# Performance work log

Hardware: AMD Instinct MI355X
Metric: run time of the kernel (lower is better)

The kernel has to match this reference:

```python
import jax, jax.numpy as jnp
import numpy as np

RARITY_ALPHA = 0.5


def _forward(obs_emb, observed_mask, lengths, avg_interval, var_prior_emb_tensor,
             rarity_W, adjI, p2s_W1, p2s_b1, p2s_W2, p2s_b2,
             Wu, bu, Wr, br, Wc, bc):
    B, T, N, D = obs_emb.shape
    I = jnp.eye(N, dtype=obs_emb.dtype)
    # hypernetwork conditioning vector per node (prior_to_state MLP); identical
    # across batch since var_prior_emb_tensor is repeated over the batch dim.
    vv = jax.nn.relu(var_prior_emb_tensor @ p2s_W1 + p2s_b1) @ p2s_W2 + p2s_b2  # [N,E]
    vv = jnp.broadcast_to(vv[None], (B, N, vv.shape[-1]))                        # [B,N,E]
    tot = observed_mask.sum(axis=1)  # var_total_obs [B,N]

    def gate(z, W, b):
        # MLP_Param: per-node weights W_n = sum_e vv[n,e]*W[e]; fused einsum avoids
        # materializing [B,N,2D+1,D].
        return jnp.einsum('bni,bne,eio->bno', z, vv, W) + jnp.einsum('bne,eo->bno', vv, b)

    def step_fn(carry, xs):
        h, out = carry
        cur_obs, m, cur_avg, step = xs  # [B,N,D], [B,N], [B,N], scalar
        rs = RARITY_ALPHA * jnp.tanh(cur_avg / (tot + 1.0))                  # [B,N]
        rmat = -rarity_W * jnp.abs(rs[:, :, None] - rs[:, None, :])          # [B,N,N]
        # adj_mask[b,i,j] = observed(b,i)*observed(b,j)  (column-set then row-zero)
        adj_mask = m[:, :, None] * m[:, None, :]
        cur_adj = adjI * (1.0 + rmat) * adj_mask * (1.0 - I) + I             # [B,N,N]
        x = jnp.concatenate([cur_obs, rs[..., None]], axis=-1)              # [B,N,D+1]
        comb = jnp.einsum('bij,bjf->bif', cur_adj,
                          jnp.concatenate([x, h], axis=-1))                  # [B,N,2D+1]
        r = jax.nn.sigmoid(gate(comb, Wr, br))
        u = jax.nn.sigmoid(gate(comb, Wu, bu))
        mm = m[..., None] > 0
        h1 = jnp.where(mm, r * h, h)                      # h[nodes_ind] = r*h[nodes_ind]
        cand = jnp.tanh(gate(jnp.concatenate([x, h1], axis=-1), Wc, bc))
        h2 = jnp.where(mm, (1.0 - u) * h1 + u * cand, h1)  # scatter back at observed nodes
        out = jnp.where((step == lengths - 1)[:, None, None], h2, out)
        return (h2, out), None

    h0 = jnp.zeros((B, N, D), obs_emb.dtype)
    xs = (obs_emb.transpose(1, 0, 2, 3), observed_mask.transpose(1, 0, 2),
          avg_interval.transpose(1, 0, 2), jnp.arange(T))
    (_, out), _ = jax.lax.scan(step_fn, (h0, jnp.zeros_like(h0)), xs)
    return out


def setup_inputs() -> dict:
    B, T, N, D, E = 32, 64, 128, 64, 5
    key = jax.random.key(0)
    ks = jax.random.split(key, 18)
    inp = {}
    inp['obs_emb'] = jax.random.normal(ks[0], (B, T, N, D), jnp.float32)
    inp['adj'] = jax.random.normal(ks[1], (N, N), jnp.float32)  # unused by forward
    inp['observed_mask'] = (jax.random.uniform(ks[2], (B, T, N)) < 0.5).astype(jnp.float32)
    inp['observed_tp'] = jax.random.uniform(ks[3], (B, T), jnp.float32)       # unused
    inp['tp_emb_tensor'] = jax.random.normal(ks[4], (B, T, 1), jnp.float32)   # unused
    inp['lengths'] = jax.random.randint(ks[5], (B,), T // 2, T + 1, jnp.int32)
    inp['avg_interval'] = jax.random.uniform(ks[6], (B, T, N), jnp.float32)
    inp['var_prior_emb_tensor'] = jax.random.normal(ks[7], (N, 768), jnp.float32)
    # learned parameters
    inp['rarity_W'] = jax.random.normal(ks[8], (N, N), jnp.float32)
    inp['adjI'] = jnp.eye(N, dtype=jnp.float32) + 0.01 * jax.random.normal(ks[9], (N, N), jnp.float32)
    inp['p2s_W1'] = 0.05 * jax.random.normal(ks[10], (768, 2 * D), jnp.float32)
    inp['p2s_b1'] = jnp.zeros((2 * D,), jnp.float32)
    inp['p2s_W2'] = 0.1 * jax.random.normal(ks[11], (2 * D, E), jnp.float32)
    inp['p2s_b2'] = jnp.zeros((E,), jnp.float32)
    inp['Wu'] = 0.1 * jax.random.normal(ks[12], (E, 2 * D + 1, D), jnp.float32)
    inp['bu'] = 0.1 * jax.random.normal(ks[13], (E, D), jnp.float32)
    inp['Wr'] = 0.1 * jax.random.normal(ks[14], (E, 2 * D + 1, D), jnp.float32)
    inp['br'] = 0.1 * jax.random.normal(ks[15], (E, D), jnp.float32)
    inp['Wc'] = 0.1 * jax.random.normal(ks[16], (E, 2 * D + 1, D), jnp.float32)
    inp['bc'] = 0.1 * jax.random.normal(ks[17], (E, D), jnp.float32)
    return inp


def reference(obs_emb, adj, observed_mask, observed_tp, tp_emb_tensor, lengths,
              avg_interval, var_prior_emb_tensor, rarity_W, adjI, p2s_W1, p2s_b1,
              p2s_W2, p2s_b2, Wu, bu, Wr, br, Wc, bc):
    # adj, observed_tp, tp_emb_tensor are accepted but never used, as in the torch code
    return _forward(obs_emb, observed_mask, lengths, avg_interval, var_prior_emb_tensor,
                    rarity_W, adjI, p2s_W1, p2s_b1, p2s_W2, p2s_b2,
                    Wu, bu, Wr, br, Wc, bc)
```

## Files before the change

### kernel.cpp

```cpp
#include <hip/hip_runtime.h>
#include <math.h>

constexpr size_t WS_VV  = 1024;
constexpr size_t WS_TOT = 2048;
constexpr size_t WS_RS  = 8192;
constexpr size_t WS_WH  = 270336;
constexpr size_t WS_WX  = 1843200;
constexpr size_t WS_BF  = 3440640;
constexpr size_t WS_H   = 3465216;
constexpr size_t WS_CH  = 3727360;
constexpr size_t WS_CX  = 3989504;
constexpr size_t WS_GXR = 8249344;
constexpr size_t WS_GXU = 12443648;
constexpr size_t WS_CXC = 16637952;

__device__ __forceinline__ float sigm(float x){ return 1.f/(1.f+expf(-x)); }

__device__ __forceinline__ float2 ld2_mall(const float* p){
  union { unsigned long long u; float2 f; } cv;
  cv.u = __hip_atomic_load((const unsigned long long*)p, __ATOMIC_RELAXED,
                           __HIP_MEMORY_SCOPE_AGENT);
  return cv.f;
}
__device__ __forceinline__ void st2_mall(float* p, float a, float b){
  union { unsigned long long u; float2 f; } cv;
  cv.f = make_float2(a, b);
  __hip_atomic_store((unsigned long long*)p, cv.u, __ATOMIC_RELAXED,
                     __HIP_MEMORY_SCOPE_AGENT);
}

__global__ void k_vv(const float* __restrict__ vpe, const float* __restrict__ W1,
                     const float* __restrict__ b1, const float* __restrict__ W2,
                     const float* __restrict__ b2, float* __restrict__ ws){
  int n = blockIdx.x, tid = threadIdx.x;
  __shared__ float hid[128];
  if (tid < 128){
    float acc = b1[tid];
    for (int k=0;k<768;k++) acc = fmaf(vpe[n*768+k], W1[k*128+tid], acc);
    hid[tid] = fmaxf(acc, 0.f);
  }
  __syncthreads();
  if (tid < 5){
    float acc = b2[tid];
    for (int h=0;h<128;h++) acc = fmaf(hid[h], W2[h*5+tid], acc);
    ws[WS_VV + n*5 + tid] = acc;
  }
}

__global__ void k_fold(const float* __restrict__ Wr, const float* __restrict__ Wu,
                       const float* __restrict__ Wc, const float* __restrict__ br,
                       const float* __restrict__ bu, const float* __restrict__ bc,
                       float* __restrict__ ws){
  int bid = blockIdx.x; int g = bid>>7; int n = bid&127;
  const float* W  = (g==0)?Wr:(g==1)?Wu:Wc;
  const float* bb = (g==0)?br:(g==1)?bu:bc;
  float v[5];
#pragma unroll
  for (int e=0;e<5;e++) v[e] = ws[WS_VV + n*5 + e];
  for (int idx=threadIdx.x; idx<129*64; idx+=256){
    int i = idx>>6, o = idx&63;
    float a = 0.f;
#pragma unroll
    for (int e=0;e<5;e++) a = fmaf(v[e], W[(e*129+i)*64+o], a);
    if (i < 65) ws[WS_WX + (size_t)(g*128+n)*4160 + i*64 + o] = a;
    else        ws[WS_WH + (size_t)(g*128+n)*4096 + (i-65)*64 + o] = a;
  }
  if (threadIdx.x < 64){
    int o = threadIdx.x; float a = 0.f;
#pragma unroll
    for (int e=0;e<5;e++) a = fmaf(v[e], bb[e*64+o], a);
    ws[WS_BF + (g*128+n)*64 + o] = a;
  }
}

__global__ void k_tot(const float* __restrict__ mask, float* __restrict__ ws){
  int id = blockIdx.x*256 + threadIdx.x;
  int b = id>>7, n = id&127;
  float s = 0.f;
  for (int t=0;t<64;t++) s += mask[(b*64+t)*128 + n];
  ws[WS_TOT + b*128 + n] = s;
}

__global__ void k_rs(const float* __restrict__ avg, float* __restrict__ ws){
  int id = blockIdx.x*256 + threadIdx.x;
  int b = id>>13, n = id&127;
  float tot = ws[WS_TOT + b*128 + n];
  ws[WS_RS + id] = 0.5f * tanhf(avg[id] / (tot + 1.f));
}

__global__ __launch_bounds__(256) void p4a(const float* __restrict__ obs,
      const float* __restrict__ mask, const float* __restrict__ adjI,
      const float* __restrict__ rW, const int* __restrict__ lengths,
      float* __restrict__ ws, int c0){
  int rc = blockIdx.x;
  int b = rc>>4, tl = rc&15, t = c0 + tl;
  if (t >= lengths[b]) return;
  int rt = b*64 + t;
  __shared__ float xt[64*68];
  __shared__ float adjh[128*68];
  __shared__ float rs_l[128], m_l[128];
  int tid = threadIdx.x;
  if (tid < 128){ rs_l[tid] = ws[WS_RS + rt*128 + tid]; m_l[tid] = mask[rt*128 + tid]; }
  __syncthreads();
  int it = tid>>3, ft = tid&7, i0 = it*4, f0 = ft*8;
  float4 aL[4], aH[4]; float a64[4];
#pragma unroll
  for (int ii=0;ii<4;ii++){ aL[ii]=make_float4(0,0,0,0); aH[ii]=make_float4(0,0,0,0); a64[ii]=0.f; }
  for (int half=0; half<2; half++){
    __syncthreads();
    int j0 = half*64;
    for (int idx=tid; idx<4096; idx+=256){
      int jl = idx>>6, f = idx&63;
      xt[jl*68+f] = obs[(size_t)rt*8192 + (j0+jl)*64 + f];
    }
    if (tid < 64) xt[tid*68+64] = rs_l[j0+tid];
    for (int idx=tid; idx<8192; idx+=256){
      int i = idx>>6, jl = idx&63, j = j0+jl;
      float a;
      if (i == j) a = 1.f;
      else {
        int gi = i*128 + j;
        float dd = fabsf(rs_l[i] - rs_l[j]);
        a = adjI[gi] * (1.f - rW[gi]*dd) * m_l[i] * m_l[j];
      }
      adjh[i*68+jl] = a;
    }
    __syncthreads();
    for (int jb=0; jb<16; jb++){
      float4 av[4];
#pragma unroll
      for (int ii=0;ii<4;ii++) av[ii] = *(const float4*)&adjh[(i0+ii)*68 + jb*4];
#pragma unroll
      for (int jj=0;jj<4;jj++){
        int jl = jb*4 + jj;
        float4 xlo = *(const float4*)&xt[jl*68 + f0];
        float4 xhi = *(const float4*)&xt[jl*68 + f0 + 4];
        float xr = xt[jl*68 + 64];
#pragma unroll
        for (int ii=0;ii<4;ii++){
          float a = (jj==0)?av[ii].x:(jj==1)?av[ii].y:(jj==2)?av[ii].z:av[ii].w;
          aL[ii].x = fmaf(a, xlo.x, aL[ii].x); aL[ii].y = fmaf(a, xlo.y, aL[ii].y);
          aL[ii].z = fmaf(a, xlo.z, aL[ii].z); aL[ii].w = fmaf(a, xlo.w, aL[ii].w);
          aH[ii].x = fmaf(a, xhi.x, aH[ii].x); aH[ii].y = fmaf(a, xhi.y, aH[ii].y);
          aH[ii].z = fmaf(a, xhi.z, aH[ii].z); aH[ii].w = fmaf(a, xhi.w, aH[ii].w);
          a64[ii] = fmaf(a, xr, a64[ii]);
        }
      }
    }
  }
#pragma unroll
  for (int ii=0;ii<4;ii++){
    int i = i0 + ii;
    size_t base = WS_CX + (size_t)i*33280 + (size_t)rc*65 + f0;
    ws[base+0]=aL[ii].x; ws[base+1]=aL[ii].y; ws[base+2]=aL[ii].z; ws[base+3]=aL[ii].w;
    ws[base+4]=aH[ii].x; ws[base+5]=aH[ii].y; ws[base+6]=aH[ii].z; ws[base+7]=aH[ii].w;
    if (ft == 0) ws[WS_CX + (size_t)i*33280 + (size_t)rc*65 + 64] = a64[ii];
  }
}

__global__ __launch_bounds__(256) void p4b(const float* __restrict__ obs,
      const int* __restrict__ lengths, float* __restrict__ ws, int c0){
  int bid = blockIdx.x;
  int g = bid >> 9; int r2 = bid & 511; int n = r2 >> 2; int tile = r2 & 3;
  __shared__ float A[128*69];
  __shared__ float Wl[65*64];
  __shared__ float bl[64];
  __shared__ int slen[32];
  int tid = threadIdx.x;
  if (tid < 32) slen[tid] = lengths[tid];
  for (int idx=tid; idx<4160; idx+=256) Wl[idx] = ws[WS_WX + (size_t)(g*128+n)*4160 + idx];
  if (tid < 64) bl[tid] = ws[WS_BF + (g*128+n)*64 + tid];
  if (g < 2){
    const float* src = &ws[WS_CX + (size_t)n*33280 + (size_t)tile*8320];
    for (int idx=tid; idx<8320; idx+=256){
      int r = idx/65, f = idx - r*65;
      A[r*69+f] = src[idx];
    }
  } else {
    for (int idx=tid; idx<8320; idx+=256){
      int r = idx/65, f = idx - r*65;
      int grow = tile*128 + r;
      int gb = grow>>4, t = c0 + (grow&15);
      float v = (f < 64) ? obs[(size_t)(gb*64+t)*8192 + n*64 + f]
                         : ws[WS_RS + (gb*64+t)*128 + n];
      A[r*69+f] = v;
    }
  }
  __syncthreads();
  int rt8 = tid>>4, dq = tid&15;
  float4 acc[8];
#pragma unroll
  for (int rr=0;rr<8;rr++) acc[rr] = make_float4(0,0,0,0);
  for (int k=0;k<65;k++){
    float4 w = *(const float4*)&Wl[k*64 + dq*4];
#pragma unroll
    for (int rr=0;rr<8;rr++){
      float a = A[(rt8*8+rr)*69 + k];
      acc[rr].x = fmaf(a,w.x,acc[rr].x); acc[rr].y = fmaf(a,w.y,acc[rr].y);
      acc[rr].z = fmaf(a,w.z,acc[rr].z); acc[rr].w = fmaf(a,w.w,acc[rr].w);
    }
  }
  float4 b4 = *(const float4*)&bl[dq*4];
  float* dst = &ws[(g==0)?WS_GXR:(g==1)?WS_GXU:WS_CXC];
#pragma unroll
  for (int rr=0;rr<8;rr++){
    int grow = tile*128 + rt8*8 + rr;
    int gb = grow>>4, gtl = grow&15;
    if (c0 + gtl < slen[gb]){
      float4 o; o.x=acc[rr].x+b4.x; o.y=acc[rr].y+b4.y; o.z=acc[rr].z+b4.z; o.w=acc[rr].w+b4.w;
      *(float4*)&dst[((size_t)(n*16+gtl)*32 + gb)*64 + dq*4] = o;
    }
  }
}

__global__ __launch_bounds__(256) void krec(const float* __restrict__ mask,
      const int* __restrict__ lengths, const float* __restrict__ adjI,
      const float* __restrict__ rWm, float* __restrict__ out, float* __restrict__ ws,
      int c0){
  unsigned* cfl = (unsigned*)ws;
  unsigned* hfl = ((unsigned*)ws) + 256;
  const int bid = blockIdx.x, tid = threadIdx.x;
  const int bA = bid>>3, sA = bid&7, ns = sA*16;
  const int nB = bid>>1, hf = bid&1, b0 = hf*16;
  __shared__ float hs[8192];
  __shared__ float adjT[2560];
  __shared__ float cT[1088];
  __shared__ float hT[1088];
  __shared__ float rs_l[128], m_l[128];
  const int lenA = lengths[bA];
  const int il = tid>>4, fq = tid&15;
  const int bb = b0 + il;
  const int slenB = lengths[bb];
  float* hbuf = &ws[WS_H];
  float* chb  = &ws[WS_CH];
  const float* wrg = &ws[WS_WH + (size_t)(0*128+nB)*4096];
  const float* wug = &ws[WS_WH + (size_t)(1*128+nB)*4096];
  const float* wcg = &ws[WS_WH + (size_t)(2*128+nB)*4096];
  float4 hst;
  { const float* hp = &hbuf[((size_t)bb*128+nB)*64 + fq*4];
    float2 lo = ld2_mall(hp), hi = ld2_mall(hp+2);
    hst = make_float4(lo.x, lo.y, hi.x, hi.y); }

  for (int t=c0; t<c0+16; t++){
    const int tl = t - c0;
    const bool aliveA = (t < lenA);
    const bool aliveB = (t < slenB);
    if (aliveA){
      if (tid < 128) rs_l[tid] = ws[WS_RS + (size_t)(bA*64+t)*128 + tid];
      else           m_l[tid-128] = mask[(size_t)(bA*64+t)*128 + (tid-128)];
    }
    __syncthreads();
    if (aliveA){
      for (int idx=tid; idx<2048; idx+=256){
        int j = idx&127, r = idx>>7, I = ns+r;
        float a;
        if (I == j) a = 1.f;
        else {
          int gi = I*128 + j;
          float dd = fabsf(rs_l[I] - rs_l[j]);
          a = adjI[gi]*(1.f - rWm[gi]*dd)*m_l[I]*m_l[j];
        }
        adjT[j*20 + r] = a;
      }
    }
    float4 arv, auv, acv; float msv = 0.f;
    if (aliveB){
      size_t gof = ((size_t)(nB*16+tl)*32 + bb)*64 + fq*4;
      arv = *(const float4*)&ws[WS_GXR + gof];
      auv = *(const float4*)&ws[WS_GXU + gof];
      acv = *(const float4*)&ws[WS_CXC + gof];
      msv = mask[(size_t)(bb*64+t)*128 + nB];
    }
    if (aliveA && t > 0 && tid < 128){
      unsigned tgt = (unsigned)t; int guard = 0;
      while (__hip_atomic_load(&hfl[tid*2 + (bA>>4)], __ATOMIC_RELAXED,
               __HIP_MEMORY_SCOPE_AGENT) < tgt && ++guard < (1<<20))
        __builtin_amdgcn_s_sleep(1);
    }
    __syncthreads();
    if (aliveA){
#pragma unroll
      for (int k2=0;k2<16;k2++){
        int p = tid + 256*k2;
        float2 v = ld2_mall(&hbuf[(size_t)bA*8192 + 2*p]);
        *(float2*)&hs[2*p] = v;
      }
    }
    __syncthreads();
    if (aliveA && tid < 128){
      int pr = tid>>4;
      float4 a0 = make_float4(0,0,0,0), a1 = a0;
#pragma unroll 4
      for (int j=0;j<128;j++){
        float2 aj = *(const float2*)&adjT[j*20 + pr*2];
        float4 h4 = *(const float4*)&hs[j*64 + fq*4];
        a0.x = fmaf(aj.x,h4.x,a0.x); a0.y = fmaf(aj.x,h4.y,a0.y);
        a0.z = fmaf(aj.x,h4.z,a0.z); a0.w = fmaf(aj.x,h4.w,a0.w);
        a1.x = fmaf(aj.y,h4.x,a1.x); a1.y = fmaf(aj.y,h4.y,a1.y);
        a1.z = fmaf(aj.y,h4.z,a1.z); a1.w = fmaf(aj.y,h4.w,a1.w);
      }
      float* cp0 = &chb[((size_t)bA*128 + ns + pr*2)*64 + fq*4];
      st2_mall(cp0,    a0.x, a0.y); st2_mall(cp0+2,  a0.z, a0.w);
      st2_mall(cp0+64, a1.x, a1.y); st2_mall(cp0+66, a1.z, a1.w);
    }
    __syncthreads();
    if (tid == 0)
      __hip_atomic_store(&cfl[sA*32 + bA], (unsigned)(t+1), __ATOMIC_RELAXED,
                         __HIP_MEMORY_SCOPE_AGENT);
    if (aliveB && fq == 0){
      unsigned tgt = (unsigned)(t+1); int guard = 0;
      while (__hip_atomic_load(&cfl[(nB>>4)*32 + bb], __ATOMIC_RELAXED,
               __HIP_MEMORY_SCOPE_AGENT) < tgt && ++guard < (1<<20))
        __builtin_amdgcn_s_sleep(1);
    }
    __syncthreads();
    if (aliveB){
      const float* cp = &chb[((size_t)bb*128 + nB)*64 + fq*4];
      float2 u = ld2_mall(cp), v = ld2_mall(cp+2);
      cT[il*68 + fq*4    ] = u.x; cT[il*68 + fq*4 + 1] = u.y;
      cT[il*68 + fq*4 + 2] = v.x; cT[il*68 + fq*4 + 3] = v.y;
    }
    __syncthreads();
    float4 uu, h1v;
    const bool ob = msv > 0.f;
    if (aliveB){
#pragma unroll 4
      for (int k=0;k<64;k++){
        float cv = cT[il*68 + k];
        float4 wr4 = *(const float4*)&wrg[k*64 + fq*4];
        float4 wu4 = *(const float4*)&wug[k*64 + fq*4];
        arv.x = fmaf(cv,wr4.x,arv.x); arv.y = fmaf(cv,wr4.y,arv.y);
        arv.z = fmaf(cv,wr4.z,arv.z); arv.w = fmaf(cv,wr4.w,arv.w);
        auv.x = fmaf(cv,wu4.x,auv.x); auv.y = fmaf(cv,wu4.y,auv.y);
        auv.z = fmaf(cv,wu4.z,auv.z); auv.w = fmaf(cv,wu4.w,auv.w);
      }
      float4 rr;
      rr.x = sigm(arv.x); rr.y = sigm(arv.y); rr.z = sigm(arv.z); rr.w = sigm(arv.w);
      uu.x = sigm(auv.x); uu.y = sigm(auv.y); uu.z = sigm(auv.z); uu.w = sigm(auv.w);
      h1v.x = ob ? rr.x*hst.x : hst.x;
      h1v.y = ob ? rr.y*hst.y : hst.y;
      h1v.z = ob ? rr.z*hst.z : hst.z;
      h1v.w = ob ? rr.w*hst.w : hst.w;
      *(float4*)&hT[il*68 + fq*4] = h1v;
    }
    __syncthreads();
    if (aliveB){
#pragma unroll 4
      for (int k=0;k<64;k++){
        float hv = hT[il*68 + k];
        float4 wc4 = *(const float4*)&wcg[k*64 + fq*4];
        acv.x = fmaf(hv,wc4.x,acv.x); acv.y = fmaf(hv,wc4.y,acv.y);
        acv.z = fmaf(hv,wc4.z,acv.z); acv.w = fmaf(hv,wc4.w,acv.w);
      }
      float4 cd, h2;
      cd.x = tanhf(acv.x); cd.y = tanhf(acv.y); cd.z = tanhf(acv.z); cd.w = tanhf(acv.w);
      h2.x = ob ? (1.f-uu.x)*h1v.x + uu.x*cd.x : h1v.x;
      h2.y = ob ? (1.f-uu.y)*h1v.y + uu.y*cd.y : h1v.y;
      h2.z = ob ? (1.f-uu.z)*h1v.z + uu.z*cd.z : h1v.z;
      h2.w = ob ? (1.f-uu.w)*h1v.w + uu.w*cd.w : h1v.w;
      hst = h2;
      float* hp = &hbuf[((size_t)bb*128 + nB)*64 + fq*4];
      st2_mall(hp,   h2.x, h2.y);
      st2_mall(hp+2, h2.z, h2.w);
      if (t == slenB-1)
        *(float4*)&out[((size_t)bb*128 + nB)*64 + fq*4] = h2;
    }
    __syncthreads();
    if (tid == 0)
      __hip_atomic_store(&hfl[nB*2 + hf], (unsigned)(t+1), __ATOMIC_RELAXED,
                         __HIP_MEMORY_SCOPE_AGENT);
  }
}

extern "C" void kernel_launch(void* const* d_in, const int* in_sizes, int n_in,
                              void* d_out, int out_size, void* d_ws, size_t ws_size,
                              hipStream_t stream){
  const float* obs  = (const float*)d_in[0];
  const float* maskp= (const float*)d_in[2];
  const int*   lens = (const int*)d_in[5];
  const float* avg  = (const float*)d_in[6];
  const float* vpe  = (const float*)d_in[7];
  const float* rW   = (const float*)d_in[8];
  const float* adjI = (const float*)d_in[9];
  const float* W1   = (const float*)d_in[10];
  const float* b1   = (const float*)d_in[11];
  const float* W2   = (const float*)d_in[12];
  const float* b2   = (const float*)d_in[13];
  const float* Wu   = (const float*)d_in[14];
  const float* bu   = (const float*)d_in[15];
  const float* Wr   = (const float*)d_in[16];
  const float* br   = (const float*)d_in[17];
  const float* Wc   = (const float*)d_in[18];
  const float* bc   = (const float*)d_in[19];
  float* out = (float*)d_out;
  float* ws  = (float*)d_ws;
  hipMemsetAsync(d_ws, 0, 4096, stream);
  hipMemsetAsync((char*)d_ws + WS_H*sizeof(float), 0, 262144*sizeof(float), stream);
  k_vv  <<<128, 256, 0, stream>>>(vpe, W1, b1, W2, b2, ws);
  k_fold<<<384, 256, 0, stream>>>(Wr, Wu, Wc, br, bu, bc, ws);
  k_tot <<<16,  256, 0, stream>>>(maskp, ws);
  k_rs  <<<1024,256, 0, stream>>>(avg, ws);
  for (int c = 0; c < 4; c++){
    int c0 = c*16;
    p4a <<<512, 256, 0, stream>>>(obs, maskp, adjI, rW, lens, ws, c0);
    p4b <<<1536,256, 0, stream>>>(obs, lens, ws, c0);
    krec<<<256, 256, 0, stream>>>(maskp, lens, adjI, rW, out, ws, c0);
  }
}
```

Before: 1.675 ms.

## Split recurrent kernel into separate aggregation and gate block roles

The persistent recurrent kernel now launches 512 blocks: the first 256 compute the adjacency aggregation and publish results, and the other 256 compute the per-node GRU gates. Each gate block caches its three per-node weight matrices in shared memory once per chunk and has each thread handle two batch rows. Stores are drained with an explicit waitcnt before the flag is published. The aim is to pipeline the two phases across blocks and cut repeated global weight reads. The cost is more blocks spinning on flags, half the threads idle in gate blocks, and a risk of deadlock if all 512 blocks are not co-resident.

```diff
diff --git a/kernel.cpp b/kernel.cpp
--- a/kernel.cpp
+++ b/kernel.cpp
@@ -220,155 +220,202 @@
   unsigned* cfl = (unsigned*)ws;
   unsigned* hfl = ((unsigned*)ws) + 256;
   const int bid = blockIdx.x, tid = threadIdx.x;
-  const int bA = bid>>3, sA = bid&7, ns = sA*16;
-  const int nB = bid>>1, hf = bid&1, b0 = hf*16;
-  __shared__ float hs[8192];
-  __shared__ float adjT[2560];
-  __shared__ float cT[1088];
-  __shared__ float hT[1088];
-  __shared__ float rs_l[128], m_l[128];
-  const int lenA = lengths[bA];
-  const int il = tid>>4, fq = tid&15;
-  const int bb = b0 + il;
-  const int slenB = lengths[bb];
+  __shared__ float smem[14848];
   float* hbuf = &ws[WS_H];
   float* chb  = &ws[WS_CH];
-  const float* wrg = &ws[WS_WH + (size_t)(0*128+nB)*4096];
-  const float* wug = &ws[WS_WH + (size_t)(1*128+nB)*4096];
-  const float* wcg = &ws[WS_WH + (size_t)(2*128+nB)*4096];
-  float4 hst;
-  { const float* hp = &hbuf[((size_t)bb*128+nB)*64 + fq*4];
-    float2 lo = ld2_mall(hp), hi = ld2_mall(hp+2);
-    hst = make_float4(lo.x, lo.y, hi.x, hi.y); }
-
-  for (int t=c0; t<c0+16; t++){
-    const int tl = t - c0;
-    const bool aliveA = (t < lenA);
-    const bool aliveB = (t < slenB);
-    if (aliveA){
-      if (tid < 128) rs_l[tid] = ws[WS_RS + (size_t)(bA*64+t)*128 + tid];
-      else           m_l[tid-128] = mask[(size_t)(bA*64+t)*128 + (tid-128)];
-    }
+
+  if (bid < 256){
+    const int bA = bid>>3, sA = bid&7, ns = sA*16;
+    float* hs   = smem;
+    float* adjT = smem + 8192;
+    float* rs_l = smem + 10752;
+    float* m_l  = smem + 10880;
+    const int lenA = lengths[bA];
+    const int pr = tid>>4, fq = tid&15;
+    for (int t=c0; t<c0+16; t++){
+      const bool aliveA = (t < lenA);
+      if (aliveA){
+        if (tid < 128) rs_l[tid] = ws[WS_RS + (size_t)(bA*64+t)*128 + tid];
+        else           m_l[tid-128] = mask[(size_t)(bA*64+t)*128 + (tid-128)];
+      }
+      __syncthreads();
+      if (aliveA){
+        for (int idx=tid; idx<2048; idx+=256){
+          int j = idx&127, r = idx>>7, I = ns+r;
+          float a;
+          if (I == j) a = 1.f;
+          else {
+            int gi = I*128 + j;
+            float dd = fabsf(rs_l[I] - rs_l[j]);
+            a = adjI[gi]*(1.f - rWm[gi]*dd)*m_l[I]*m_l[j];
+          }
+          adjT[j*20 + r] = a;
+        }
+        if (t > 0 && tid < 128){
+          unsigned tgt = (unsigned)t; int guard = 0;
+          while (__hip_atomic_load(&hfl[tid*2 + (bA>>4)], __ATOMIC_RELAXED,
+                   __HIP_MEMORY_SCOPE_AGENT) < tgt && ++guard < (1<<20))
+            __builtin_amdgcn_s_sleep(1);
+        }
+      }
+      __syncthreads();
+      if (aliveA){
+#pragma unroll
+        for (int k2=0;k2<16;k2++){
+          int p = tid + 256*k2;
+          float2 v = ld2_mall(&hbuf[(size_t)bA*8192 + 2*p]);
+          *(float2*)&hs[2*p] = v;
+        }
+      }
+      __syncthreads();
+      if (aliveA && tid < 128){
+        float4 a0 = make_float4(0,0,0,0), a1 = a0;
+#pragma unroll 4
+        for (int j=0;j<128;j++){
+          float2 aj = *(const float2*)&adjT[j*20 + pr*2];
+          float4 h4 = *(const float4*)&hs[j*64 + fq*4];
+          a0.x = fmaf(aj.x,h4.x,a0.x); a0.y = fmaf(aj.x,h4.y,a0.y);
+          a0.z = fmaf(aj.x,h4.z,a0.z); a0.w = fmaf(aj.x,h4.w,a0.w);
+          a1.x = fmaf(aj.y,h4.x,a1.x); a1.y = fmaf(aj.y,h4.y,a1.y);
+          a1.z = fmaf(aj.y,h4.z,a1.z); a1.w = fmaf(aj.y,h4.w,a1.w);
+        }
+        float* cp0 = &chb[((size_t)bA*128 + ns + pr*2)*64 + fq*4];
+        st2_mall(cp0,    a0.x, a0.y); st2_mall(cp0+2,  a0.z, a0.w);
+        st2_mall(cp0+64, a1.x, a1.y); st2_mall(cp0+66, a1.z, a1.w);
+      }
+      asm volatile("s_waitcnt vmcnt(0)" ::: "memory");
+      __syncthreads();
+      if (tid == 0)
+        __hip_atomic_store(&cfl[sA*32 + bA], (unsigned)(t+1), __ATOMIC_RELAXED,
+                           __HIP_MEMORY_SCOPE_AGENT);
+    }
+  } else {
+    const int nB = (bid-256)>>1, hf = (bid-256)&1, b0 = hf*16;
+    float* wR = smem;
+    float* wU = smem + 4096;
+    float* wC = smem + 8192;
+    float* cT = smem + 12288;
+    float* hT = smem + 13568;
+    for (int idx=tid; idx<3072; idx+=256){
+      int g = idx>>10, r = idx&1023;
+      *(float4*)&smem[g*4096 + r*4] =
+        *(const float4*)&ws[WS_WH + (size_t)(g*128+nB)*4096 + (size_t)r*4];
+    }
+    const int p = tid>>4, fq = tid&15;
+    const int bb0 = b0 + ((p&7)*2), bb1 = bb0 + 1;
+    const int sl0 = lengths[bb0], sl1 = lengths[bb1];
+    float4 h0, h1p;
+    { const float* q0 = &hbuf[((size_t)bb0*128+nB)*64 + fq*4];
+      const float* q1 = &hbuf[((size_t)bb1*128+nB)*64 + fq*4];
+      float2 a = ld2_mall(q0), b = ld2_mall(q0+2);
+      float2 c = ld2_mall(q1), d = ld2_mall(q1+2);
+      h0 = make_float4(a.x,a.y,b.x,b.y); h1p = make_float4(c.x,c.y,d.x,d.y); }
     __syncthreads();
-    if (aliveA){
-      for (int idx=tid; idx<2048; idx+=256){
-        int j = idx&127, r = idx>>7, I = ns+r;
-        float a;
-        if (I == j) a = 1.f;
-        else {
-          int gi = I*128 + j;
-          float dd = fabsf(rs_l[I] - rs_l[j]);
-          a = adjI[gi]*(1.f - rWm[gi]*dd)*m_l[I]*m_l[j];
-        }
-        adjT[j*20 + r] = a;
-      }
-    }
-    float4 arv, auv, acv; float msv = 0.f;
-    if (aliveB){
-      size_t gof = ((size_t)(nB*16+tl)*32 + bb)*64 + fq*4;
-      arv = *(const float4*)&ws[WS_GXR + gof];
-      auv = *(const float4*)&ws[WS_GXU + gof];
-      acv = *(const float4*)&ws[WS_CXC + gof];
-      msv = mask[(size_t)(bb*64+t)*128 + nB];
-    }
-    if (aliveA && t > 0 && tid < 128){
-      unsigned tgt = (unsigned)t; int guard = 0;
-      while (__hip_atomic_load(&hfl[tid*2 + (bA>>4)], __ATOMIC_RELAXED,
-               __HIP_MEMORY_SCOPE_AGENT) < tgt && ++guard < (1<<20))
-        __builtin_amdgcn_s_sleep(1);
-    }
-    __syncthreads();
-    if (aliveA){
-#pragma unroll
-      for (int k2=0;k2<16;k2++){
-        int p = tid + 256*k2;
-        float2 v = ld2_mall(&hbuf[(size_t)bA*8192 + 2*p]);
-        *(float2*)&hs[2*p] = v;
-      }
-    }
-    __syncthreads();
-    if (aliveA && tid < 128){
-      int pr = tid>>4;
-      float4 a0 = make_float4(0,0,0,0), a1 = a0;
+    for (int t=c0; t<c0+16; t++){
+      const int tl = t - c0;
+      const bool al0 = (t < sl0), al1 = (t < sl1);
+      float4 xr0,xr1,xu0,xu1,xc0,xc1; float m0=0.f, m1=0.f;
+      if (tid < 128){
+        size_t g0 = ((size_t)(nB*16+tl)*32 + bb0)*64 + fq*4;
+        size_t g1 = ((size_t)(nB*16+tl)*32 + bb1)*64 + fq*4;
+        xr0 = *(const float4*)&ws[WS_GXR + g0]; xr1 = *(const float4*)&ws[WS_GXR + g1];
+        xu0 = *(const float4*)&ws[WS_GXU + g0]; xu1 = *(const float4*)&ws[WS_GXU + g1];
+        xc0 = *(const float4*)&ws[WS_CXC + g0]; xc1 = *(const float4*)&ws[WS_CXC + g1];
+        m0 = mask[(size_t)(bb0*64+t)*128 + nB];
+        m1 = mask[(size_t)(bb1*64+t)*128 + nB];
+      }
+      if (tid < 16){
+        unsigned tgt = (unsigned)(t+1); int guard = 0;
+        while (__hip_atomic_load(&cfl[(nB>>4)*32 + b0 + tid], __ATOMIC_RELAXED,
+                 __HIP_MEMORY_SCOPE_AGENT) < tgt && ++guard < (1<<20))
+          __builtin_amdgcn_s_sleep(1);
+      }
+      __syncthreads();
+      {
+        int bi = tid>>4, fg = tid&15, f0 = fg*4;
+        const float* cp = &chb[((size_t)(b0+bi)*128 + nB)*64 + f0];
+        float2 u = ld2_mall(cp), v = ld2_mall(cp+2);
+        cT[(f0  )*20 + bi] = u.x; cT[(f0+1)*20 + bi] = u.y;
+        cT[(f0+2)*20 + bi] = v.x; cT[(f0+3)*20 + bi] = v.y;
+      }
+      __syncthreads();
+      float4 uu0, uu1, h1a, h1b;
+      const bool ob0 = m0 > 0.f, ob1 = m1 > 0.f;
+      if (tid < 128){
+        float4 ar0=xr0, ar1=xr1, au0=xu0, au1=xu1;
 #pragma unroll 4
-      for (int j=0;j<128;j++){
-        float2 aj = *(const float2*)&adjT[j*20 + pr*2];
-        float4 h4 = *(const float4*)&hs[j*64 + fq*4];
-        a0.x = fmaf(aj.x,h4.x,a0.x); a0.y = fmaf(aj.x,h4.y,a0.y);
-        a0.z = fmaf(aj.x,h4.z,a0.z); a0.w = fmaf(aj.x,h4.w,a0.w);
-        a1.x = fmaf(aj.y,h4.x,a1.x); a1.y = fmaf(aj.y,h4.y,a1.y);
-        a1.z = fmaf(aj.y,h4.z,a1.z); a1.w = fmaf(aj.y,h4.w,a1.w);
-      }
-      float* cp0 = &chb[((size_t)bA*128 + ns + pr*2)*64 + fq*4];
-      st2_mall(cp0,    a0.x, a0.y); st2_mall(cp0+2,  a0.z, a0.w);
-      st2_mall(cp0+64, a1.x, a1.y); st2_mall(cp0+66, a1.z, a1.w);
-    }
-    __syncthreads();
-    if (tid == 0)
-      __hip_atomic_store(&cfl[sA*32 + bA], (unsigned)(t+1), __ATOMIC_RELAXED,
-                         __HIP_MEMORY_SCOPE_AGENT);
-    if (aliveB && fq == 0){
-      unsigned tgt = (unsigned)(t+1); int guard = 0;
-      while (__hip_atomic_load(&cfl[(nB>>4)*32 + bb], __ATOMIC_RELAXED,
-               __HIP_MEMORY_SCOPE_AGENT) < tgt && ++guard < (1<<20))
-        __builtin_amdgcn_s_sleep(1);
-    }
-    __syncthreads();
-    if (aliveB){
-      const float* cp = &chb[((size_t)bb*128 + nB)*64 + fq*4];
-      float2 u = ld2_mall(cp), v = ld2_mall(cp+2);
-      cT[il*68 + fq*4    ] = u.x; cT[il*68 + fq*4 + 1] = u.y;
-      cT[il*68 + fq*4 + 2] = v.x; cT[il*68 + fq*4 + 3] = v.y;
-    }
-    __syncthreads();
-    float4 uu, h1v;
-    const bool ob = msv > 0.f;
-    if (aliveB){
+        for (int k=0;k<64;k++){
+          float2 c2 = *(const float2*)&cT[k*20 + (p&7)*2];
+          float4 wr4 = *(const float4*)&wR[k*64 + fq*4];
+          float4 wu4 = *(const float4*)&wU[k*64 + fq*4];
+          ar0.x = fmaf(c2.x,wr4.x,ar0.x); ar0.y = fmaf(c2.x,wr4.y,ar0.y);
+          ar0.z = fmaf(c2.x,wr4.z,ar0.z); ar0.w = fmaf(c2.x,wr4.w,ar0.w);
+          ar1.x = fmaf(c2.y,wr4.x,ar1.x); ar1.y = fmaf(c2.y,wr4.y,ar1.y);
+          ar1.z = fmaf(c2.y,wr4.z,ar1.z); ar1.w = fmaf(c2.y,wr4.w,ar1.w);
+          au0.x = fmaf(c2.x,wu4.x,au0.x); au0.y = fmaf(c2.x,wu4.y,au0.y);
+          au0.z = fmaf(c2.x,wu4.z,au0.z); au0.w = fmaf(c2.x,wu4.w,au0.w);
+          au1.x = fmaf(c2.y,wu4.x,au1.x); au1.y = fmaf(c2.y,wu4.y,au1.y);
+          au1.z = fmaf(c2.y,wu4.z,au1.z); au1.w = fmaf(c2.y,wu4.w,au1.w);
+        }
+        float4 r0, r1;
+        r0.x=sigm(ar0.x); r0.y=sigm(ar0.y); r0.z=sigm(ar0.z); r0.w=sigm(ar0.w);
+        r1.x=sigm(ar1.x); r1.y=sigm(ar1.y); r1.z=sigm(ar1.z); r1.w=sigm(ar1.w);
+        uu0.x=sigm(au0.x); uu0.y=sigm(au0.y); uu0.z=sigm(au0.z); uu0.w=sigm(au0.w);
+        uu1.x=sigm(au1.x); uu1.y=sigm(au1.y); uu1.z=sigm(au1.z); uu1.w=sigm(au1.w);
+        bool q0 = al0 && ob0, q1 = al1 && ob1;
+        h1a.x = q0 ? r0.x*h0.x : h0.x;  h1a.y = q0 ? r0.y*h0.y : h0.y;
+        h1a.z = q0 ? r0.z*h0.z : h0.z;  h1a.w = q0 ? r0.w*h0.w : h0.w;
+        h1b.x = q1 ? r1.x*h1p.x : h1p.x; h1b.y = q1 ? r1.y*h1p.y : h1p.y;
+        h1b.z = q1 ? r1.z*h1p.z : h1p.z; h1b.w = q1 ? r1.w*h1p.w : h1p.w;
+        const float* pa = (const float*)&h1a;
+        const float* pb = (const float*)&h1b;
+#pragma unroll
+        for (int q=0;q<4;q++)
+          *(float2*)&hT[(fq*4+q)*20 + (p&7)*2] = make_float2(pa[q], pb[q]);
+      }
+      __syncthreads();
+      if (tid < 128){
+        float4 ac0=xc0, ac1=xc1;
 #pragma unroll 4
-      for (int k=0;k<64;k++){
-        float cv = cT[il*68 + k];
-        float4 wr4 = *(const float4*)&wrg[k*64 + fq*4];
-        float4 wu4 = *(const float4*)&wug[k*64 + fq*4];
-        arv.x = fmaf(cv,wr4.x,arv.x); arv.y = fmaf(cv,wr4.y,arv.y);
-        arv.z = fmaf(cv,wr4.z,arv.z); arv.w = fmaf(cv,wr4.w,arv.w);
-        auv.x = fmaf(cv,wu4.x,auv.x); auv.y = fmaf(cv,wu4.y,auv.y);
-        auv.z = fmaf(cv,wu4.z,auv.z); auv.w = fmaf(cv,wu4.w,auv.w);
-      }
-      float4 rr;
-      rr.x = sigm(arv.x); rr.y = sigm(arv.y); rr.z = sigm(arv.z); rr.w = sigm(arv.w);
-      uu.x = sigm(auv.x); uu.y = sigm(auv.y); uu.z = sigm(auv.z); uu.w = sigm(auv.w);
-      h1v.x = ob ? rr.x*hst.x : hst.x;
-      h1v.y = ob ? rr.y*hst.y : hst.y;
-      h1v.z = ob ? rr.z*hst.z : hst.z;
-      h1v.w = ob ? rr.w*hst.w : hst.w;
-      *(float4*)&hT[il*68 + fq*4] = h1v;
-    }
-    __syncthreads();
-    if (aliveB){
-#pragma unroll 4
-      for (int k=0;k<64;k++){
-        float hv = hT[il*68 + k];
-        float4 wc4 = *(const float4*)&wcg[k*64 + fq*4];
-        acv.x = fmaf(hv,wc4.x,acv.x); acv.y = fmaf(hv,wc4.y,acv.y);
-        acv.z = fmaf(hv,wc4.z,acv.z); acv.w = fmaf(hv,wc4.w,acv.w);
-      }
-      float4 cd, h2;
-      cd.x = tanhf(acv.x); cd.y = tanhf(acv.y); cd.z = tanhf(acv.z); cd.w = tanhf(acv.w);
-      h2.x = ob ? (1.f-uu.x)*h1v.x + uu.x*cd.x : h1v.x;
-      h2.y = ob ? (1.f-uu.y)*h1v.y + uu.y*cd.y : h1v.y;
-      h2.z = ob ? (1.f-uu.z)*h1v.z + uu.z*cd.z : h1v.z;
-      h2.w = ob ? (1.f-uu.w)*h1v.w + uu.w*cd.w : h1v.w;
-      hst = h2;
-      float* hp = &hbuf[((size_t)bb*128 + nB)*64 + fq*4];
-      st2_mall(hp,   h2.x, h2.y);
-      st2_mall(hp+2, h2.z, h2.w);
-      if (t == slenB-1)
-        *(float4*)&out[((size_t)bb*128 + nB)*64 + fq*4] = h2;
-    }
-    __syncthreads();
-    if (tid == 0)
-      __hip_atomic_store(&hfl[nB*2 + hf], (unsigned)(t+1), __ATOMIC_RELAXED,
-                         __HIP_MEMORY_SCOPE_AGENT);
+        for (int k=0;k<64;k++){
+          float2 hh = *(const float2*)&hT[k*20 + (p&7)*2];
+          float4 wc4 = *(const float4*)&wC[k*64 + fq*4];
+          ac0.x = fmaf(hh.x,wc4.x,ac0.x); ac0.y = fmaf(hh.x,wc4.y,ac0.y);
+          ac0.z = fmaf(hh.x,wc4.z,ac0.z); ac0.w = fmaf(hh.x,wc4.w,ac0.w);
+          ac1.x = fmaf(hh.y,wc4.x,ac1.x); ac1.y = fmaf(hh.y,wc4.y,ac1.y);
+          ac1.z = fmaf(hh.y,wc4.z,ac1.z); ac1.w = fmaf(hh.y,wc4.w,ac1.w);
+        }
+        if (al0){
+          float4 cd, h2;
+          cd.x=tanhf(ac0.x); cd.y=tanhf(ac0.y); cd.z=tanhf(ac0.z); cd.w=tanhf(ac0.w);
+          h2.x = ob0 ? (1.f-uu0.x)*h1a.x + uu0.x*cd.x : h1a.x;
+          h2.y = ob0 ? (1.f-uu0.y)*h1a.y + uu0.y*cd.y : h1a.y;
+          h2.z = ob0 ? (1.f-uu0.z)*h1a.z + uu0.z*cd.z : h1a.z;
+          h2.w = ob0 ? (1.f-uu0.w)*h1a.w + uu0.w*cd.w : h1a.w;
+          h0 = h2;
+          float* hp = &hbuf[((size_t)bb0*128 + nB)*64 + fq*4];
+          st2_mall(hp, h2.x, h2.y); st2_mall(hp+2, h2.z, h2.w);
+          if (t == sl0-1) *(float4*)&out[((size_t)bb0*128 + nB)*64 + fq*4] = h2;
+        }
+        if (al1){
+          float4 cd, h2;
+          cd.x=tanhf(ac1.x); cd.y=tanhf(ac1.y); cd.z=tanhf(ac1.z); cd.w=tanhf(ac1.w);
+          h2.x = ob1 ? (1.f-uu1.x)*h1b.x + uu1.x*cd.x : h1b.x;
+          h2.y = ob1 ? (1.f-uu1.y)*h1b.y + uu1.y*cd.y : h1b.y;
+          h2.z = ob1 ? (1.f-uu1.z)*h1b.z + uu1.z*cd.z : h1b.z;
+          h2.w = ob1 ? (1.f-uu1.w)*h1b.w + uu1.w*cd.w : h1b.w;
+          h1p = h2;
+          float* hp = &hbuf[((size_t)bb1*128 + nB)*64 + fq*4];
+          st2_mall(hp, h2.x, h2.y); st2_mall(hp+2, h2.z, h2.w);
+          if (t == sl1-1) *(float4*)&out[((size_t)bb1*128 + nB)*64 + fq*4] = h2;
+        }
+      }
+      asm volatile("s_waitcnt vmcnt(0)" ::: "memory");
+      __syncthreads();
+      if (tid == 0)
+        __hip_atomic_store(&hfl[nB*2 + hf], (unsigned)(t+1), __ATOMIC_RELAXED,
+                           __HIP_MEMORY_SCOPE_AGENT);
+    }
   }
 }
 
@@ -404,6 +451,6 @@
     int c0 = c*16;
     p4a <<<512, 256, 0, stream>>>(obs, maskp, adjI, rW, lens, ws, c0);
     p4b <<<1536,256, 0, stream>>>(obs, lens, ws, c0);
-    krec<<<256, 256, 0, stream>>>(maskp, lens, adjI, rW, out, ws, c0);
-  }
-}
+    krec<<<512, 256, 0, stream>>>(maskp, lens, adjI, rW, out, ws, c0);
+  }
+}
```

Result: slower. 1.773 ms (+5.8%).

## Split recurrent kernel into producer/consumer blocks with fine-grained per-batch flags

Applied to the files above, without the earlier changes.

The recurrent kernel now launches 512 blocks. 256 of them compute only the adjacency-times-h aggregation, with adjI and rarity weights staged in LDS. The other 256 compute only the gate update, with the three folded weight matrices cached in LDS. Flags now sit per batch and per node instead of being coarse, and gate blocks advance each batch row independently as soon as its aggregated input is ready, so lockstep waits across the batch go away. This adds more resident blocks and spin-polling. It relies on all 512 blocks being co-resident to avoid deadlock.

```diff
diff --git a/kernel.cpp b/kernel.cpp
--- a/kernel.cpp
+++ b/kernel.cpp
@@ -13,6 +13,7 @@
 constexpr size_t WS_GXR = 8249344;
 constexpr size_t WS_GXU = 12443648;
 constexpr size_t WS_CXC = 16637952;
+constexpr size_t WS_FLG = 20832256;
 
 __device__ __forceinline__ float sigm(float x){ return 1.f/(1.f+expf(-x)); }
 
@@ -27,6 +28,12 @@
   cv.f = make_float2(a, b);
   __hip_atomic_store((unsigned long long*)p, cv.u, __ATOMIC_RELAXED,
                      __HIP_MEMORY_SCOPE_AGENT);
+}
+__device__ __forceinline__ unsigned ldflag(const unsigned* p){
+  return __hip_atomic_load(p, __ATOMIC_RELAXED, __HIP_MEMORY_SCOPE_AGENT);
+}
+__device__ __forceinline__ void stflag(unsigned* p, unsigned v){
+  __hip_atomic_store(p, v, __ATOMIC_RELAXED, __HIP_MEMORY_SCOPE_AGENT);
 }
 
 __global__ void k_vv(const float* __restrict__ vpe, const float* __restrict__ W1,
@@ -217,158 +224,196 @@
       const int* __restrict__ lengths, const float* __restrict__ adjI,
       const float* __restrict__ rWm, float* __restrict__ out, float* __restrict__ ws,
       int c0){
-  unsigned* cfl = (unsigned*)ws;
-  unsigned* hfl = ((unsigned*)ws) + 256;
+  unsigned* cfl  = (unsigned*)(ws + WS_FLG);
+  unsigned* hfl2 = ((unsigned*)(ws + WS_FLG)) + 256;
   const int bid = blockIdx.x, tid = threadIdx.x;
-  const int bA = bid>>3, sA = bid&7, ns = sA*16;
-  const int nB = bid>>1, hf = bid&1, b0 = hf*16;
-  __shared__ float hs[8192];
-  __shared__ float adjT[2560];
-  __shared__ float cT[1088];
-  __shared__ float hT[1088];
-  __shared__ float rs_l[128], m_l[128];
-  const int lenA = lengths[bA];
-  const int il = tid>>4, fq = tid&15;
-  const int bb = b0 + il;
-  const int slenB = lengths[bb];
+  __shared__ float smem[15104];
   float* hbuf = &ws[WS_H];
   float* chb  = &ws[WS_CH];
-  const float* wrg = &ws[WS_WH + (size_t)(0*128+nB)*4096];
-  const float* wug = &ws[WS_WH + (size_t)(1*128+nB)*4096];
-  const float* wcg = &ws[WS_WH + (size_t)(2*128+nB)*4096];
-  float4 hst;
-  { const float* hp = &hbuf[((size_t)bb*128+nB)*64 + fq*4];
-    float2 lo = ld2_mall(hp), hi = ld2_mall(hp+2);
-    hst = make_float4(lo.x, lo.y, hi.x, hi.y); }
-
-  for (int t=c0; t<c0+16; t++){
-    const int tl = t - c0;
-    const bool aliveA = (t < lenA);
-    const bool aliveB = (t < slenB);
-    if (aliveA){
+
+  if (bid < 256){
+    const int bA = bid>>3, sA = bid&7, ns = sA*16;
+    float* hs   = smem;
+    float* adjT = smem + 8192;
+    float* adjS = smem + 10752;
+    float* rWS  = smem + 12800;
+    float* rs_l = smem + 14848;
+    float* m_l  = smem + 14976;
+    const int lenA = lengths[bA];
+    if (c0 >= lenA) return;
+    for (int idx=tid; idx<2048; idx+=256){
+      int gi = (ns + (idx>>7))*128 + (idx&127);
+      adjS[idx] = adjI[gi];
+      rWS[idx]  = rWm[gi];
+    }
+    const int pr = tid>>4, fq = tid&15;
+    const int tEnd = (lenA < c0+16) ? lenA : (c0+16);
+    __syncthreads();
+    for (int t=c0; t<tEnd; t++){
       if (tid < 128) rs_l[tid] = ws[WS_RS + (size_t)(bA*64+t)*128 + tid];
       else           m_l[tid-128] = mask[(size_t)(bA*64+t)*128 + (tid-128)];
-    }
-    __syncthreads();
-    if (aliveA){
+      __syncthreads();
       for (int idx=tid; idx<2048; idx+=256){
-        int j = idx&127, r = idx>>7, I = ns+r;
+        int r = idx>>7, j = idx&127, I = ns+r;
         float a;
         if (I == j) a = 1.f;
         else {
-          int gi = I*128 + j;
           float dd = fabsf(rs_l[I] - rs_l[j]);
-          a = adjI[gi]*(1.f - rWm[gi]*dd)*m_l[I]*m_l[j];
+          a = adjS[idx]*(1.f - rWS[idx]*dd)*m_l[I]*m_l[j];
         }
         adjT[j*20 + r] = a;
       }
-    }
-    float4 arv, auv, acv; float msv = 0.f;
-    if (aliveB){
-      size_t gof = ((size_t)(nB*16+tl)*32 + bb)*64 + fq*4;
-      arv = *(const float4*)&ws[WS_GXR + gof];
-      auv = *(const float4*)&ws[WS_GXU + gof];
-      acv = *(const float4*)&ws[WS_CXC + gof];
-      msv = mask[(size_t)(bb*64+t)*128 + nB];
-    }
-    if (aliveA && t > 0 && tid < 128){
-      unsigned tgt = (unsigned)t; int guard = 0;
-      while (__hip_atomic_load(&hfl[tid*2 + (bA>>4)], __ATOMIC_RELAXED,
-               __HIP_MEMORY_SCOPE_AGENT) < tgt && ++guard < (1<<20))
-        __builtin_amdgcn_s_sleep(1);
-    }
-    __syncthreads();
-    if (aliveA){
+      if (tid < 128){
+        unsigned tgt = (unsigned)t; int guard = 0;
+        while (ldflag(&hfl2[bA*128 + tid]) < tgt && ++guard < (1<<20))
+          __builtin_amdgcn_s_sleep(1);
+      }
+      __syncthreads();
 #pragma unroll
       for (int k2=0;k2<16;k2++){
         int p = tid + 256*k2;
         float2 v = ld2_mall(&hbuf[(size_t)bA*8192 + 2*p]);
         *(float2*)&hs[2*p] = v;
       }
-    }
+      __syncthreads();
+      {
+        float4 acc = make_float4(0,0,0,0);
+#pragma unroll 4
+        for (int j=0;j<128;j++){
+          float aj = adjT[j*20 + pr];
+          float4 h4 = *(const float4*)&hs[j*64 + fq*4];
+          acc.x = fmaf(aj,h4.x,acc.x); acc.y = fmaf(aj,h4.y,acc.y);
+          acc.z = fmaf(aj,h4.z,acc.z); acc.w = fmaf(aj,h4.w,acc.w);
+        }
+        float* cp = &chb[((size_t)bA*128 + ns + pr)*64 + fq*4];
+        st2_mall(cp,   acc.x, acc.y);
+        st2_mall(cp+2, acc.z, acc.w);
+      }
+      asm volatile("s_waitcnt vmcnt(0)" ::: "memory");
+      __syncthreads();
+      if (tid == 0)
+        stflag(&cfl[bA*8 + sA], (unsigned)(t+1));
+    }
+  } else {
+    const int nB = (bid-256)>>1, hf = (bid-256)&1, b0 = hf*16;
+    float* wR = smem;
+    float* wU = smem + 4096;
+    float* wC = smem + 8192;
+    float* cT = smem + 12288;
+    float* hT = cT + 1088;
+    int* done = (int*)(hT + 1088);
+    int* tgt  = done + 16;
+    int* mword= tgt + 16;
+    int* remw = mword + 1;
+    for (int idx=tid; idx<3072; idx+=256){
+      int g = idx>>10, r = idx&1023;
+      *(float4*)&smem[g*4096 + r*4] =
+        *(const float4*)&ws[WS_WH + (size_t)(g*128+nB)*4096 + (size_t)r*4];
+    }
+    const int bi = tid>>4, fq = tid&15;
+    const int bb = b0 + bi;
+    const int slenB = lengths[bb];
+    const int sIdx = nB>>4;
+    if (tid < 16){
+      int sl = lengths[b0 + tid];
+      int tg = sl - c0; if (tg < 0) tg = 0; if (tg > 16) tg = 16;
+      tgt[tid] = tg; done[tid] = 0;
+    }
+    if (tid == 0) *remw = 0;
     __syncthreads();
-    if (aliveA && tid < 128){
-      int pr = tid>>4;
-      float4 a0 = make_float4(0,0,0,0), a1 = a0;
+    if (tid < 16) atomicAdd(remw, tgt[tid]);
+    float4 hst;
+    { const float* hp = &hbuf[((size_t)bb*128+nB)*64 + fq*4];
+      float2 lo = ld2_mall(hp), hi = ld2_mall(hp+2);
+      hst = make_float4(lo.x, lo.y, hi.x, hi.y); }
+    __syncthreads();
+    int rem = *remw;
+    for (int pass=0; pass<6000 && rem>0; pass++){
+      int dn = done[bi];
+      int t  = c0 + dn;
+      bool maybe = (dn < tgt[bi]);
+      float4 xr, xu, xc; float mv = 0.f;
+      if (maybe){
+        size_t gof = ((size_t)(nB*16+dn)*32 + bb)*64 + fq*4;
+        xr = *(const float4*)&ws[WS_GXR + gof];
+        xu = *(const float4*)&ws[WS_GXU + gof];
+        xc = *(const float4*)&ws[WS_CXC + gof];
+        mv = mask[(size_t)(bb*64+t)*128 + nB];
+      }
+      if (tid == 0) *mword = 0;
+      __syncthreads();
+      if (tid < 16){
+        int d2 = done[tid];
+        bool rdy = (d2 < tgt[tid]);
+        if (rdy)
+          rdy = (ldflag(&cfl[(b0+tid)*8 + sIdx]) >= (unsigned)(c0 + d2 + 1));
+        if (rdy) atomicOr(mword, 1<<tid);
+      }
+      __syncthreads();
+      unsigned msk = (unsigned)*mword;
+      if (msk == 0){ __builtin_amdgcn_s_sleep(4); continue; }
+      const bool act = (msk>>bi) & 1;
+      if (act){
+        const float* cp = &chb[((size_t)bb*128 + nB)*64 + fq*4];
+        float2 u = ld2_mall(cp), v = ld2_mall(cp+2);
+        *(float4*)&cT[bi*68 + fq*4] = make_float4(u.x,u.y,v.x,v.y);
+      }
+      __syncthreads();
+      float4 uu, h1v; const bool ob = mv > 0.f;
+      if (act){
+        float4 ar = xr, au = xu;
 #pragma unroll 4
-      for (int j=0;j<128;j++){
-        float2 aj = *(const float2*)&adjT[j*20 + pr*2];
-        float4 h4 = *(const float4*)&hs[j*64 + fq*4];
-        a0.x = fmaf(aj.x,h4.x,a0.x); a0.y = fmaf(aj.x,h4.y,a0.y);
-        a0.z = fmaf(aj.x,h4.z,a0.z); a0.w = fmaf(aj.x,h4.w,a0.w);
-        a1.x = fmaf(aj.y,h4.x,a1.x); a1.y = fmaf(aj.y,h4.y,a1.y);
-        a1.z = fmaf(aj.y,h4.z,a1.z); a1.w = fmaf(aj.y,h4.w,a1.w);
-      }
-      float* cp0 = &chb[((size_t)bA*128 + ns + pr*2)*64 + fq*4];
-      st2_mall(cp0,    a0.x, a0.y); st2_mall(cp0+2,  a0.z, a0.w);
-      st2_mall(cp0+64, a1.x, a1.y); st2_mall(cp0+66, a1.z, a1.w);
-    }
-    __syncthreads();
-    if (tid == 0)
-      __hip_atomic_store(&cfl[sA*32 + bA], (unsigned)(t+1), __ATOMIC_RELAXED,
-                         __HIP_MEMORY_SCOPE_AGENT);
-    if (aliveB && fq == 0){
-      unsigned tgt = (unsigned)(t+1); int guard = 0;
-      while (__hip_atomic_load(&cfl[(nB>>4)*32 + bb], __ATOMIC_RELAXED,
-               __HIP_MEMORY_SCOPE_AGENT) < tgt && ++guard < (1<<20))
-        __builtin_amdgcn_s_sleep(1);
-    }
-    __syncthreads();
-    if (aliveB){
-      const float* cp = &chb[((size_t)bb*128 + nB)*64 + fq*4];
-      float2 u = ld2_mall(cp), v = ld2_mall(cp+2);
-      cT[il*68 + fq*4    ] = u.x; cT[il*68 + fq*4 + 1] = u.y;
-      cT[il*68 + fq*4 + 2] = v.x; cT[il*68 + fq*4 + 3] = v.y;
-    }
-    __syncthreads();
-    float4 uu, h1v;
-    const bool ob = msv > 0.f;
-    if (aliveB){
+        for (int k=0;k<64;k++){
+          float cv = cT[bi*68 + k];
+          float4 wr4 = *(const float4*)&wR[k*64 + fq*4];
+          float4 wu4 = *(const float4*)&wU[k*64 + fq*4];
+          ar.x = fmaf(cv,wr4.x,ar.x); ar.y = fmaf(cv,wr4.y,ar.y);
+          ar.z = fmaf(cv,wr4.z,ar.z); ar.w = fmaf(cv,wr4.w,ar.w);
+          au.x = fmaf(cv,wu4.x,au.x); au.y = fmaf(cv,wu4.y,au.y);
+          au.z = fmaf(cv,wu4.z,au.z); au.w = fmaf(cv,wu4.w,au.w);
+        }
+        float4 rr;
+        rr.x = sigm(ar.x); rr.y = sigm(ar.y); rr.z = sigm(ar.z); rr.w = sigm(ar.w);
+        uu.x = sigm(au.x); uu.y = sigm(au.y); uu.z = sigm(au.z); uu.w = sigm(au.w);
+        h1v.x = ob ? rr.x*hst.x : hst.x;
+        h1v.y = ob ? rr.y*hst.y : hst.y;
+        h1v.z = ob ? rr.z*hst.z : hst.z;
+        h1v.w = ob ? rr.w*hst.w : hst.w;
+        *(float4*)&hT[bi*68 + fq*4] = h1v;
+      }
+      __syncthreads();
+      if (act){
+        float4 ac = xc;
 #pragma unroll 4
-      for (int k=0;k<64;k++){
-        float cv = cT[il*68 + k];
-        float4 wr4 = *(const float4*)&wrg[k*64 + fq*4];
-        float4 wu4 = *(const float4*)&wug[k*64 + fq*4];
-        arv.x = fmaf(cv,wr4.x,arv.x); arv.y = fmaf(cv,wr4.y,arv.y);
-        arv.z = fmaf(cv,wr4.z,arv.z); arv.w = fmaf(cv,wr4.w,arv.w);
-        auv.x = fmaf(cv,wu4.x,auv.x); auv.y = fmaf(cv,wu4.y,auv.y);
-        auv.z = fmaf(cv,wu4.z,auv.z); auv.w = fmaf(cv,wu4.w,auv.w);
-      }
-      float4 rr;
-      rr.x = sigm(arv.x); rr.y = sigm(arv.y); rr.z = sigm(arv.z); rr.w = sigm(arv.w);
-      uu.x = sigm(auv.x); uu.y = sigm(auv.y); uu.z = sigm(auv.z); uu.w = sigm(auv.w);
-      h1v.x = ob ? rr.x*hst.x : hst.x;
-      h1v.y = ob ? rr.y*hst.y : hst.y;
-      h1v.z = ob ? rr.z*hst.z : hst.z;
-      h1v.w = ob ? rr.w*hst.w : hst.w;
-      *(float4*)&hT[il*68 + fq*4] = h1v;
-    }
-    __syncthreads();
-    if (aliveB){
-#pragma unroll 4
-      for (int k=0;k<64;k++){
-        float hv = hT[il*68 + k];
-        float4 wc4 = *(const float4*)&wcg[k*64 + fq*4];
-        acv.x = fmaf(hv,wc4.x,acv.x); acv.y = fmaf(hv,wc4.y,acv.y);
-        acv.z = fmaf(hv,wc4.z,acv.z); acv.w = fmaf(hv,wc4.w,acv.w);
-      }
-      float4 cd, h2;
-      cd.x = tanhf(acv.x); cd.y = tanhf(acv.y); cd.z = tanhf(acv.z); cd.w = tanhf(acv.w);
-      h2.x = ob ? (1.f-uu.x)*h1v.x + uu.x*cd.x : h1v.x;
-      h2.y = ob ? (1.f-uu.y)*h1v.y + uu.y*cd.y : h1v.y;
-      h2.z = ob ? (1.f-uu.z)*h1v.z + uu.z*cd.z : h1v.z;
-      h2.w = ob ? (1.f-uu.w)*h1v.w + uu.w*cd.w : h1v.w;
-      hst = h2;
-      float* hp = &hbuf[((size_t)bb*128 + nB)*64 + fq*4];
-      st2_mall(hp,   h2.x, h2.y);
-      st2_mall(hp+2, h2.z, h2.w);
-      if (t == slenB-1)
-        *(float4*)&out[((size_t)bb*128 + nB)*64 + fq*4] = h2;
-    }
-    __syncthreads();
-    if (tid == 0)
-      __hip_atomic_store(&hfl[nB*2 + hf], (unsigned)(t+1), __ATOMIC_RELAXED,
-                         __HIP_MEMORY_SCOPE_AGENT);
+        for (int k=0;k<64;k++){
+          float hv = hT[bi*68 + k];
+          float4 wc4 = *(const float4*)&wC[k*64 + fq*4];
+          ac.x = fmaf(hv,wc4.x,ac.x); ac.y = fmaf(hv,wc4.y,ac.y);
+          ac.z = fmaf(hv,wc4.z,ac.z); ac.w = fmaf(hv,wc4.w,ac.w);
+        }
+        float4 cd, h2;
+        cd.x = tanhf(ac.x); cd.y = tanhf(ac.y); cd.z = tanhf(ac.z); cd.w = tanhf(ac.w);
+        h2.x = ob ? (1.f-uu.x)*h1v.x + uu.x*cd.x : h1v.x;
+        h2.y = ob ? (1.f-uu.y)*h1v.y + uu.y*cd.y : h1v.y;
+        h2.z = ob ? (1.f-uu.z)*h1v.z + uu.z*cd.z : h1v.z;
+        h2.w = ob ? (1.f-uu.w)*h1v.w + uu.w*cd.w : h1v.w;
+        hst = h2;
+        float* hp = &hbuf[((size_t)bb*128 + nB)*64 + fq*4];
+        st2_mall(hp,   h2.x, h2.y);
+        st2_mall(hp+2, h2.z, h2.w);
+        if (t == slenB-1)
+          *(float4*)&out[((size_t)bb*128 + nB)*64 + fq*4] = h2;
+      }
+      asm volatile("s_waitcnt vmcnt(0)" ::: "memory");
+      __syncthreads();
+      if (tid < 16 && ((msk>>tid)&1)){
+        done[tid] += 1;
+        stflag(&hfl2[(b0+tid)*128 + nB], (unsigned)(c0 + done[tid]));
+        atomicSub(remw, 1);
+      }
+      __syncthreads();
+      rem = *remw;
+    }
   }
 }
 
@@ -394,7 +439,7 @@
   const float* bc   = (const float*)d_in[19];
   float* out = (float*)d_out;
   float* ws  = (float*)d_ws;
-  hipMemsetAsync(d_ws, 0, 4096, stream);
+  hipMemsetAsync((char*)d_ws + WS_FLG*sizeof(float), 0, 4352*sizeof(unsigned), stream);
   hipMemsetAsync((char*)d_ws + WS_H*sizeof(float), 0, 262144*sizeof(float), stream);
   k_vv  <<<128, 256, 0, stream>>>(vpe, W1, b1, W2, b2, ws);
   k_fold<<<384, 256, 0, stream>>>(Wr, Wu, Wc, br, bu, bc, ws);
@@ -404,6 +449,6 @@
     int c0 = c*16;
     p4a <<<512, 256, 0, stream>>>(obs, maskp, adjI, rW, lens, ws, c0);
     p4b <<<1536,256, 0, stream>>>(obs, lens, ws, c0);
-    krec<<<256, 256, 0, stream>>>(maskp, lens, adjI, rW, out, ws, c0);
-  }
-}
+    krec<<<512, 256, 0, stream>>>(maskp, lens, adjI, rW, out, ws, c0);
+  }
+}
```

Result: slower. 1.828 ms (+9.1%).
